# Optimization experiments

Hardware: AMD Instinct MI355X
Metric: run time of the kernel (lower is better)

## Reference

```python
import jax, jax.numpy as jnp
import numpy as np

HIDDEN = 2048
N_HEADS = 16
N_KV_HEADS = 4
HEAD_DIM = HIDDEN // N_HEADS  # 128
ROPE_THETA = 10000.0
BATCH = 2
SEQ = 2048


def setup_inputs() -> dict:
    key = jax.random.key(0)
    k1, k2, k3, k4, k5 = jax.random.split(key, 5)
    s = 0.02
    return {
        "hidden_states": jax.random.normal(k1, (BATCH, SEQ, HIDDEN), dtype=jnp.float32),
        "attention_mask": jnp.zeros((BATCH, 1, 1, SEQ), dtype=jnp.float32),
        "Wq": jax.random.normal(k2, (HIDDEN, N_HEADS * HEAD_DIM), dtype=jnp.float32) * s,
        "Wk": jax.random.normal(k3, (HIDDEN, N_KV_HEADS * HEAD_DIM), dtype=jnp.float32) * s,
        "Wv": jax.random.normal(k4, (HIDDEN, N_KV_HEADS * HEAD_DIM), dtype=jnp.float32) * s,
        "Wo": jax.random.normal(k5, (N_HEADS * HEAD_DIM, HIDDEN), dtype=jnp.float32) * s,
    }


def _rope_cos_sin(seq_len, dtype):
    inv_freq = 1.0 / (ROPE_THETA ** (jnp.arange(0, HEAD_DIM, 2, dtype=jnp.float32) / HEAD_DIM))
    t = jnp.arange(seq_len, dtype=jnp.float32)
    freqs = t[:, None] * inv_freq[None, :]            # [S, D/2]
    emb = jnp.concatenate([freqs, freqs], axis=-1)    # [S, D]
    cos = jnp.cos(emb)[None, None, :, :].astype(dtype)  # [1,1,S,D]
    sin = jnp.sin(emb)[None, None, :, :].astype(dtype)
    return cos, sin


def _apply_rope(x, cos, sin):
    # x: [B,H,S,D]; faithful to torch code: rotated = cat((-x[...,1::2], x[...,::2]), -1)
    x1 = x[..., ::2]
    x2 = x[..., 1::2]
    rotated = jnp.concatenate([-x2, x1], axis=-1)
    return x * cos + rotated * sin


def reference(hidden_states, attention_mask, Wq, Wk, Wv, Wo):
    B, S, _ = hidden_states.shape
    scale = HEAD_DIM ** -0.5

    q = (hidden_states @ Wq).reshape(B, S, N_HEADS, HEAD_DIM).transpose(0, 2, 1, 3)      # [B,H,S,D]
    k = (hidden_states @ Wk).reshape(B, S, N_KV_HEADS, HEAD_DIM).transpose(0, 2, 1, 3)   # [B,KV,S,D]
    v = (hidden_states @ Wv).reshape(B, S, N_KV_HEADS, HEAD_DIM).transpose(0, 2, 1, 3)

    cos, sin = _rope_cos_sin(S, hidden_states.dtype)
    q = _apply_rope(q, cos, sin)
    k = _apply_rope(k, cos, sin)

    rep = N_HEADS // N_KV_HEADS
    k = jnp.repeat(k, rep, axis=1)  # [B,H,S,D]
    v = jnp.repeat(v, rep, axis=1)

    scores = jnp.einsum("bhqd,bhkd->bhqk", q, k) * scale  # [B,H,S,S]
    causal = jnp.tril(jnp.ones((S, S), dtype=bool))[None, None]
    scores = jnp.where(causal, scores, -jnp.inf)
    scores = scores + attention_mask  # additive float mask, broadcast [B,1,1,S]

    attn = jax.nn.softmax(scores, axis=-1)
    out = jnp.einsum("bhqk,bhkd->bhqd", attn, v)           # [B,H,S,D]
    out = out.transpose(0, 2, 1, 3).reshape(B, S, N_HEADS * HEAD_DIM)
    return out @ Wo
```

## Files before the change

kernel.cpp:

```cpp
#include <hip/hip_runtime.h>
#include <hip/hip_bf16.h>

#define BATCH 2
#define SEQ   2048
#define NH    16
#define NKV   4
#define HD    128
#define KDIM  2048
#define MROWS 4096
#define NQKV  3072

typedef __attribute__((ext_vector_type(8))) short  s16x8;
typedef __attribute__((ext_vector_type(4))) short  s16x4;
typedef __attribute__((ext_vector_type(4))) float  f32x4;
typedef __attribute__((ext_vector_type(8))) __bf16 b16x8;

#define BARRIER_LDS() do { \
    asm volatile("s_waitcnt lgkmcnt(0)" ::: "memory"); \
    __builtin_amdgcn_s_barrier(); \
  } while (0)

__device__ __forceinline__ unsigned short f2bf(float f) {
  __hip_bfloat16 h = __float2bfloat16(f);
  return *reinterpret_cast<unsigned short*>(&h);
}
__device__ __forceinline__ float bf2f(unsigned short h) {
  union { unsigned int u; float f; } x; x.u = ((unsigned int)h) << 16;
  return x.f;
}

__device__ __forceinline__ unsigned pack2_trunc(float hif, float lof) {
  unsigned r, sel = 0x07060302u;
  asm("v_perm_b32 %0, %1, %2, %3" : "=v"(r) : "v"(hif), "v"(lof), "v"(sel));
  return r;
}
__device__ __forceinline__ float max3f(float a, float b, float c) {
  float r;
  asm("v_max3_f32 %0, %1, %2, %3" : "=v"(r) : "v"(a), "v"(b), "v"(c));
  return r;
}

__device__ __forceinline__ f32x4 MFMA16(s16x8 a, s16x8 b, f32x4 c) {
  return __builtin_amdgcn_mfma_f32_16x16x32_bf16(
      __builtin_bit_cast(b16x8, a), __builtin_bit_cast(b16x8, b), c, 0, 0, 0);
}

__device__ __forceinline__ void gload_lds16(const void* g, void* lds) {
  __builtin_amdgcn_global_load_lds(
      (const __attribute__((address_space(1))) void*)g,
      (__attribute__((address_space(3))) void*)lds, 16, 0, 0);
}

__global__ __launch_bounds__(256) void prep_all(
    const float* __restrict__ hidden,
    const float* __restrict__ Wq, const float* __restrict__ Wk,
    const float* __restrict__ Wv, const float* __restrict__ Wo,
    const float* __restrict__ mask,
    unsigned short* __restrict__ Ab, unsigned short* __restrict__ BT,
    unsigned short* __restrict__ WoT, float* __restrict__ tbl,
    float* __restrict__ maskS) {
  __shared__ float tile[32][33];
  int bid = blockIdx.x;
  if (bid < 10240) {
    int sub = bid % 160, ky = bid / 160;
    const float* W; unsigned short* WT; int Nd, nb;
    if (sub < 64)       { W = Wq; WT = BT;                       Nd = 2048; nb = sub; }
    else if (sub < 80)  { W = Wk; WT = BT + (size_t)2048 * KDIM; Nd = 512;  nb = sub - 64; }
    else if (sub < 96)  { W = Wv; WT = BT + (size_t)2560 * KDIM; Nd = 512;  nb = sub - 80; }
    else                { W = Wo; WT = WoT;                      Nd = 2048; nb = sub - 96; }
    int n0 = nb * 32, k0 = ky * 32;
    int tx = threadIdx.x & 31, ty = threadIdx.x >> 5;
#pragma unroll
    for (int i = 0; i < 4; ++i)
      tile[ty + i * 8][tx] = W[(size_t)(k0 + ty + i * 8) * Nd + n0 + tx];
    __syncthreads();
#pragma unroll
    for (int i = 0; i < 4; ++i)
      WT[(size_t)(n0 + ty + i * 8) * KDIM + k0 + tx] = f2bf(tile[tx][ty + i * 8]);
  } else if (bid < 14336) {
    int i = (bid - 10240) * 256 + threadIdx.x;
    const float4 a = ((const float4*)hidden)[2 * i];
    const float4 b = ((const float4*)hidden)[2 * i + 1];
    s16x8 o;
    o[0] = (short)f2bf(a.x); o[1] = (short)f2bf(a.y);
    o[2] = (short)f2bf(a.z); o[3] = (short)f2bf(a.w);
    o[4] = (short)f2bf(b.x); o[5] = (short)f2bf(b.y);
    o[6] = (short)f2bf(b.z); o[7] = (short)f2bf(b.w);
    ((s16x8*)Ab)[i] = o;
  } else if (bid < 14848) {
    int i = (bid - 14336) * 256 + threadIdx.x;
    int s = i >> 6, j = i & 63;
    float inv = powf(10000.0f, -(float)(2 * j) * (1.0f / 128.0f));
    float f = (float)s * inv;
    tbl[2 * i]     = cosf(f);
    tbl[2 * i + 1] = sinf(f);
  } else {
    int i = (bid - 14848) * 256 + threadIdx.x;
    maskS[i] = mask[i] * 1.44269504088896f;
  }
}

__global__ __launch_bounds__(512, 2) void gemm_qkv(
    const unsigned short* __restrict__ A, const unsigned short* __restrict__ BT,
    const float* __restrict__ tbl,
    unsigned short* __restrict__ Qo, unsigned short* __restrict__ Ko,
    unsigned short* __restrict__ Vo) {
  __shared__ __align__(16) unsigned short lds_[66560];
#define RING(buf, ab) (lds_ + (((buf) * 2 + (ab)) << 13))
  int tid = threadIdx.x, lane = tid & 63;
  int w = tid >> 6, wm = w >> 2, wn = w & 3;
  int lin = blockIdx.x;
  int swz = (lin & 7) * 24 + (lin >> 3);
  int bx = swz % 12, by = swz / 12;
  int m0 = by * 256, n0 = bx * 256;
  int fr = lane & 15, cg4 = lane >> 4, rg4 = (lane >> 4) * 4;

  int rS1 = tid >> 2,        cS1 = (tid & 3) ^ (rS1 & 3);
  int t2  = tid + 512;
  int rS2 = t2 >> 2,         cS2 = (t2 & 3) ^ (rS2 & 3);

  f32x4 acc[8][4] = {};

#pragma unroll
  for (int kt = 0; kt < 2; ++kt) {
    gload_lds16(A + (size_t)(m0 + rS1) * KDIM + kt * 32 + cS1 * 8,
                (char*)RING(kt, 0) + (size_t)tid * 16);
    gload_lds16(A + (size_t)(m0 + rS2) * KDIM + kt * 32 + cS2 * 8,
                (char*)RING(kt, 0) + (size_t)t2 * 16);
    gload_lds16(BT + (size_t)(n0 + rS1) * KDIM + kt * 32 + cS1 * 8,
                (char*)RING(kt, 1) + (size_t)tid * 16);
    gload_lds16(BT + (size_t)(n0 + rS2) * KDIM + kt * 32 + cS2 * 8,
                (char*)RING(kt, 1) + (size_t)t2 * 16);
  }

  const int NK = KDIM / 32;
  for (int kt = 0; kt < NK; ++kt) {
    int buf = kt & 3;
    if (kt == NK - 1) asm volatile("s_waitcnt vmcnt(0)" ::: "memory");
    else              asm volatile("s_waitcnt vmcnt(4)" ::: "memory");
    __builtin_amdgcn_s_barrier();

    const unsigned short* lA = RING(buf, 0);
    const unsigned short* lB = RING(buf, 1);
    s16x8 bfr[4], afr[4];
#pragma unroll
    for (int nf = 0; nf < 4; ++nf) {
      int rb = wn * 64 + nf * 16 + fr;
      bfr[nf] = *(const s16x8*)(lB + rb * 32 + (cg4 ^ (rb & 3)) * 8);
    }
#pragma unroll
    for (int mf = 0; mf < 4; ++mf) {
      int ra = wm * 128 + mf * 16 + fr;
      afr[mf] = *(const s16x8*)(lA + ra * 32 + (cg4 ^ (ra & 3)) * 8);
    }
    if (kt + 2 < NK) {
      int nb = (kt + 2) & 3, ko = (kt + 2) * 32;
      gload_lds16(A + (size_t)(m0 + rS1) * KDIM + ko + cS1 * 8,
                  (char*)RING(nb, 0) + (size_t)tid * 16);
      gload_lds16(A + (size_t)(m0 + rS2) * KDIM + ko + cS2 * 8,
                  (char*)RING(nb, 0) + (size_t)t2 * 16);
    }
    __builtin_amdgcn_s_setprio(1);
#pragma unroll
    for (int mf = 0; mf < 4; ++mf)
#pragma unroll
      for (int nf = 0; nf < 4; ++nf)
        acc[mf][nf] = MFMA16(afr[mf], bfr[nf], acc[mf][nf]);
    __builtin_amdgcn_s_setprio(0);
#pragma unroll
    for (int mf = 0; mf < 4; ++mf) {
      int ra = wm * 128 + (mf + 4) * 16 + fr;
      afr[mf] = *(const s16x8*)(lA + ra * 32 + (cg4 ^ (ra & 3)) * 8);
    }
    if (kt + 2 < NK) {
      int nb = (kt + 2) & 3, ko = (kt + 2) * 32;
      gload_lds16(BT + (size_t)(n0 + rS1) * KDIM + ko + cS1 * 8,
                  (char*)RING(nb, 1) + (size_t)tid * 16);
      gload_lds16(BT + (size_t)(n0 + rS2) * KDIM + ko + cS2 * 8,
                  (char*)RING(nb, 1) + (size_t)t2 * 16);
    }
    __builtin_amdgcn_s_setprio(1);
#pragma unroll
    for (int mf = 0; mf < 4; ++mf)
#pragma unroll
      for (int nf = 0; nf < 4; ++nf)
        acc[mf + 4][nf] = MFMA16(afr[mf], bfr[nf], acc[mf + 4][nf]);
    __builtin_amdgcn_s_setprio(0);
  }

  if (bx < 10) {
    BARRIER_LDS();
    unsigned short* sc_ = lds_;
#pragma unroll
    for (int mf = 0; mf < 8; ++mf)
#pragma unroll
      for (int nf = 0; nf < 4; ++nf)
#pragma unroll
        for (int r = 0; r < 4; ++r)
          sc_[(wm * 128 + mf * 16 + rg4 + r) * 260 + wn * 64 + nf * 16 + fr] =
              f2bf(acc[mf][nf][r]);
    BARRIER_LDS();

#pragma unroll
    for (int i = 0; i < 8; ++i) {
      int t = tid + 512 * i;
      int row = t >> 4, rem = t & 15;
      int hl = rem >> 3, j0 = (rem & 7) * 8;
      int grow = m0 + row, bb = grow >> 11, ss = grow & 2047;
      const unsigned short* xb = sc_ + row * 260 + hl * 128;
      s16x8 xj  = *(const s16x8*)(xb + j0);
      s16x8 xj6 = *(const s16x8*)(xb + 64 + j0);
      s16x8 x2a = *(const s16x8*)(xb + 2 * j0);
      s16x8 x2b = *(const s16x8*)(xb + 2 * j0 + 8);
      const float* tb = tbl + ((size_t)ss * 64 + j0) * 2;
      union { float4 v[4]; float a[16]; } cs;
      cs.v[0] = *(const float4*)(tb);
      cs.v[1] = *(const float4*)(tb + 4);
      cs.v[2] = *(const float4*)(tb + 8);
      cs.v[3] = *(const float4*)(tb + 12);
      s16x8 o0, o1;
#pragma unroll
      for (int k = 0; k < 8; ++k) {
        float c  = cs.a[2 * k];
        float sn = cs.a[2 * k + 1];
        float xjf  = bf2f((unsigned short)xj[k]);
        float xj6f = bf2f((unsigned short)xj6[k]);
        float x2j  = (2 * k < 8) ? bf2f((unsigned short)x2a[2 * k])
                                 : bf2f((unsigned short)x2b[2 * k - 8]);
        float x2j1 = (2 * k + 1 < 8) ? bf2f((unsigned short)x2a[2 * k + 1])
                                     : bf2f((unsigned short)x2b[2 * k + 1 - 8]);
        o0[k] = (short)f2bf(xjf * c - x2j1 * sn);
        o1[k] = (short)f2bf(xj6f * c + x2j * sn);
      }
      unsigned short* dstp;
      if (bx < 8) {
        int hh = bx * 2 + hl;
        dstp = Qo + ((size_t)(bb * NH + hh) * SEQ + ss) * HD;
      } else {
        int kvh = (bx - 8) * 2 + hl;
        dstp = Ko + ((size_t)(bb * NKV + kvh) * SEQ + ss) * HD;
      }
      *(s16x8*)(dstp + j0)      = o0;
      *(s16x8*)(dstp + 64 + j0) = o1;
    }
  } else {
    int rbase = m0 + wm * 128 + rg4;
#pragma unroll
    for (int nf = 0; nf < 4; ++nf) {
      int gn = n0 + wn * 64 + nf * 16 + fr;
      int c = gn - 2560, kvh = c >> 7, d = c & 127;
#pragma unroll
      for (int mf = 0; mf < 8; ++mf) {
        int grow0 = rbase + mf * 16;
        int bb = grow0 >> 11, ss = grow0 & 2047;
        s16x4 pk;
#pragma unroll
        for (int r = 0; r < 4; ++r) pk[r] = (short)f2bf(acc[mf][nf][r]);
        *(s16x4*)(Vo + ((size_t)(bb * NKV + kvh) * HD + d) * SEQ + ss) = pk;
      }
    }
  }
#undef RING
}

__global__ __launch_bounds__(512, 1) void gemm_out(
    const unsigned short* __restrict__ A, const unsigned short* __restrict__ BT,
    float* __restrict__ C) {
  __shared__ __align__(16) unsigned short ldsA[4][8192];
  __shared__ __align__(16) unsigned short ldsB[4][4096];
  int tid = threadIdx.x, lane = tid & 63;
  int w = tid >> 6, wm = w >> 2, wn = w & 3;
  int lin = blockIdx.x;
  int swz = (lin & 7) * 32 + (lin >> 3);
  int bx = swz % 16, by = swz / 16;
  int m0 = by * 256, n0 = bx * 128;
  int fr = lane & 15, cg4 = lane >> 4, rg4 = (lane >> 4) * 4;

  int rS1 = tid >> 2,  cS1 = (tid & 3) ^ (rS1 & 3);
  int t2  = tid + 512;
  int rS2 = t2 >> 2,   cS2 = (t2 & 3) ^ (rS2 & 3);
  int rB  = tid >> 2,  cB  = (tid & 3) ^ (rB & 3);

  f32x4 acc[8][2] = {};

#pragma unroll
  for (int kt = 0; kt < 2; ++kt) {
    gload_lds16(A + (size_t)(m0 + rS1) * KDIM + kt * 32 + cS1 * 8,
                (char*)&ldsA[kt][0] + (size_t)tid * 16);
    gload_lds16(A + (size_t)(m0 + rS2) * KDIM + kt * 32 + cS2 * 8,
                (char*)&ldsA[kt][0] + (size_t)t2 * 16);
    gload_lds16(BT + (size_t)(n0 + rB) * KDIM + kt * 32 + cB * 8,
                (char*)&ldsB[kt][0] + (size_t)tid * 16);
  }

  const int NK = KDIM / 32;
  for (int kt = 0; kt < NK; ++kt) {
    int buf = kt & 3;
    if (kt == NK - 1) asm volatile("s_waitcnt vmcnt(0)" ::: "memory");
    else              asm volatile("s_waitcnt vmcnt(3)" ::: "memory");
    __builtin_amdgcn_s_barrier();

    const unsigned short* lA = &ldsA[buf][0];
    const unsigned short* lB = &ldsB[buf][0];
    s16x8 bfr[2], afr[4];
#pragma unroll
    for (int nf = 0; nf < 2; ++nf) {
      int rb = wn * 32 + nf * 16 + fr;
      bfr[nf] = *(const s16x8*)(lB + rb * 32 + (cg4 ^ (rb & 3)) * 8);
    }
#pragma unroll
    for (int mf = 0; mf < 4; ++mf) {
      int ra = wm * 128 + mf * 16 + fr;
      afr[mf] = *(const s16x8*)(lA + ra * 32 + (cg4 ^ (ra & 3)) * 8);
    }
    if (kt + 2 < NK) {
      int nb = (kt + 2) & 3, ko = (kt + 2) * 32;
      gload_lds16(A + (size_t)(m0 + rS1) * KDIM + ko + cS1 * 8,
                  (char*)&ldsA[nb][0] + (size_t)tid * 16);
      gload_lds16(A + (size_t)(m0 + rS2) * KDIM + ko + cS2 * 8,
                  (char*)&ldsA[nb][0] + (size_t)t2 * 16);
    }
    __builtin_amdgcn_s_setprio(1);
#pragma unroll
    for (int mf = 0; mf < 4; ++mf)
#pragma unroll
      for (int nf = 0; nf < 2; ++nf)
        acc[mf][nf] = MFMA16(afr[mf], bfr[nf], acc[mf][nf]);
    __builtin_amdgcn_s_setprio(0);
#pragma unroll
    for (int mf = 0; mf < 4; ++mf) {
      int ra = wm * 128 + (mf + 4) * 16 + fr;
      afr[mf] = *(const s16x8*)(lA + ra * 32 + (cg4 ^ (ra & 3)) * 8);
    }
    if (kt + 2 < NK) {
      int nb = (kt + 2) & 3, ko = (kt + 2) * 32;
      gload_lds16(BT + (size_t)(n0 + rB) * KDIM + ko + cB * 8,
                  (char*)&ldsB[nb][0] + (size_t)tid * 16);
    }
    __builtin_amdgcn_s_setprio(1);
#pragma unroll
    for (int mf = 0; mf < 4; ++mf)
#pragma unroll
      for (int nf = 0; nf < 2; ++nf)
        acc[mf + 4][nf] = MFMA16(afr[mf], bfr[nf], acc[mf + 4][nf]);
    __builtin_amdgcn_s_setprio(0);
  }

  int rbase = m0 + wm * 128 + rg4;
#pragma unroll
  for (int nf = 0; nf < 2; ++nf) {
    int gn = n0 + wn * 32 + nf * 16 + fr;
#pragma unroll
    for (int mf = 0; mf < 8; ++mf)
#pragma unroll
      for (int r = 0; r < 4; ++r)
        C[(size_t)(rbase + mf * 16 + r) * 2048 + gn] = acc[mf][nf][r];
  }
}

__global__ __launch_bounds__(256, 2) void attn_fwd(
    const unsigned short* __restrict__ Q, const unsigned short* __restrict__ K,
    const unsigned short* __restrict__ VT, const float* __restrict__ maskS,
    unsigned short* __restrict__ O) {
  __shared__ __align__(16) unsigned short kt_[2][64][136];
  __shared__ __align__(16) unsigned short vt_[2][128][68];
  __shared__ __align__(16) unsigned short pt_[4][16][36];

  int tid = threadIdx.x, lane = tid & 63, w = tid >> 6;
  int l = blockIdx.x;
  int grp = l & 7, slot = l >> 3;
  int hloc = slot & 3, qt = 31 - (slot >> 2);
  int b = grp >> 2, kvh = grp & 3, h = kvh * 4 + hloc;
  int qbase = qt * 64;
  int qw = qbase + w * 16;
  int fr = lane & 15, g = lane >> 4, kg = g * 8, rg = g * 4;

  const unsigned short* Qb = Q + (size_t)(b * NH + h) * SEQ * HD;
  const unsigned short* Kb = K + (size_t)(b * NKV + kvh) * SEQ * HD;
  const unsigned short* Vb = VT + (size_t)(b * NKV + kvh) * HD * SEQ;
  const float* mb = maskS + (size_t)b * SEQ;

  int krow = tid >> 4, kpos = (tid & 15) * 8;
  const float sc2 = 0.12751744584812722f;
  int bS = b * SEQ;
  int ntiles = qt + 1;

  s16x8 aq[4];
#pragma unroll
  for (int dc = 0; dc < 4; ++dc)
    aq[dc] = *(const s16x8*)(Qb + (size_t)(qw + fr) * HD + dc * 32 + kg);

  f32x4 oacc[8] = {};
  float m_r = -3e38f, l_r = 0.f;

  s16x8 kreg[4], vreg[4];
#pragma unroll
  for (int i = 0; i < 4; ++i)
    kreg[i] = *(const s16x8*)(Kb + (size_t)(krow + i * 16) * HD + kpos);
#pragma unroll
  for (int i = 0; i < 4; ++i) {
    int c = tid + 256 * i;
    vreg[i] = *(const s16x8*)(Vb + (size_t)(c >> 3) * SEQ + (c & 7) * 8);
  }
#pragma unroll
  for (int i = 0; i < 4; ++i)
    *(s16x8*)(&kt_[0][krow + i * 16][kpos]) = kreg[i];
#pragma unroll
  for (int i = 0; i < 4; ++i) {
    int c = tid + 256 * i;
    *(s16x8*)(&vt_[0][c >> 3][(c & 7) * 8]) = vreg[i];
  }
  if (ntiles > 1) {
#pragma unroll
    for (int i = 0; i < 4; ++i)
      kreg[i] = *(const s16x8*)(Kb + (size_t)(64 + krow + i * 16) * HD + kpos);
#pragma unroll
    for (int i = 0; i < 4; ++i) {
      int c = tid + 256 * i;
      vreg[i] = *(const s16x8*)(Vb + (size_t)(c >> 3) * SEQ + 64 + (c & 7) * 8);
    }
  }
  BARRIER_LDS();

  for (int t = 0; t < ntiles; ++t) {
    int kv0 = t * 64;
    int cur = t & 1;
    bool diag = (t == qt);

    if (t + 1 < ntiles) {
#pragma unroll
      for (int i = 0; i < 4; ++i)
        *(s16x8*)(&kt_[cur ^ 1][krow + i * 16][kpos]) = kreg[i];
#pragma unroll
      for (int i = 0; i < 4; ++i) {
        int c = tid + 256 * i;
        *(s16x8*)(&vt_[cur ^ 1][c >> 3][(c & 7) * 8]) = vreg[i];
      }
      if (t + 2 < ntiles) {
#pragma unroll
        for (int i = 0; i < 4; ++i)
          kreg[i] = *(const s16x8*)(Kb + (size_t)(kv0 + 128 + krow + i * 16) * HD + kpos);
#pragma unroll
        for (int i = 0; i < 4; ++i) {
          int c = tid + 256 * i;
          vreg[i] = *(const s16x8*)(Vb + (size_t)(c >> 3) * SEQ + kv0 + 128 + (c & 7) * 8);
        }
      }
    }

    f32x4 sf[4];
    __builtin_amdgcn_s_setprio(1);
#pragma unroll
    for (int mk = 0; mk < 4; ++mk) {
      s16x8 ak[4];
#pragma unroll
      for (int dc = 0; dc < 4; ++dc)
        ak[dc] = *(const s16x8*)(&kt_[cur][mk * 16 + fr][dc * 32 + kg]);
      sf[mk] = f32x4{0.f, 0.f, 0.f, 0.f};
#pragma unroll
      for (int dc = 0; dc < 4; ++dc)
        sf[mk] = MFMA16(ak[dc], aq[dc], sf[mk]);
    }
    __builtin_amdgcn_s_setprio(0);

#pragma unroll
    for (int mk = 0; mk < 4; ++mk) {
      float4 mv = *(const float4*)(mb + kv0 + mk * 16 + rg);
      float mvr[4] = {mv.x, mv.y, mv.z, mv.w};
      if (diag) {
#pragma unroll
        for (int r = 0; r < 4; ++r) {
          int kv = kv0 + mk * 16 + rg + r;
          float v = sf[mk][r] * sc2 + mvr[r];
          sf[mk][r] = (kv <= qw + fr) ? v : -3e38f;
        }
      } else {
#pragma unroll
        for (int r = 0; r < 4; ++r)
          sf[mk][r] = sf[mk][r] * sc2 + mvr[r];
      }
    }

    float m0_ = max3f(sf[0][0], sf[0][1], sf[0][2]);
    float m1_ = max3f(sf[0][3], sf[1][0], sf[1][1]);
    float m2_ = max3f(sf[1][2], sf[1][3], sf[2][0]);
    float m3_ = max3f(sf[2][1], sf[2][2], sf[2][3]);
    float m4_ = max3f(sf[3][0], sf[3][1], sf[3][2]);
    float ma_ = max3f(m0_, m1_, m2_);
    float mb_ = max3f(m3_, m4_, sf[3][3]);
    float pm = fmaxf(ma_, mb_);
    pm = fmaxf(pm, __shfl_xor(pm, 16, 64));
    pm = fmaxf(pm, __shfl_xor(pm, 32, 64));
    if (!__all(pm - m_r <= 8.0f)) {
      float mo = m_r;
      float mn = fmaxf(mo, pm);
      float al = exp2f(mo - mn);
      m_r = mn;
      l_r *= al;
#pragma unroll
      for (int r = 0; r < 4; ++r) {
        float ar = __shfl(al, rg + r, 16);
#pragma unroll
        for (int od = 0; od < 8; ++od) oacc[od][r] *= ar;
      }
    }
    float rs = 0.f;
#pragma unroll
    for (int mk = 0; mk < 4; ++mk)
#pragma unroll
      for (int r = 0; r < 4; ++r) {
        float ppv = exp2f(sf[mk][r] - m_r);
        sf[mk][r] = ppv;
        rs += ppv;
      }
    rs += __shfl_xor(rs, 16, 64);
    rs += __shfl_xor(rs, 32, 64);
    l_r += rs;

#pragma unroll
    for (int kk = 0; kk < 2; ++kk) {
#pragma unroll
      for (int mh = 0; mh < 2; ++mh) {
        int mk = kk * 2 + mh;
        unsigned w0 = pack2_trunc(sf[mk][1], sf[mk][0]);
        unsigned w1 = pack2_trunc(sf[mk][3], sf[mk][2]);
        uint2 pk2; pk2.x = w0; pk2.y = w1;
        *(uint2*)(&pt_[w][fr][mh * 16 + rg]) = pk2;
      }
      s16x8 ap = *(const s16x8*)(&pt_[w][fr][kg]);
      __builtin_amdgcn_s_setprio(1);
#pragma unroll
      for (int od = 0; od < 8; ++od) {
        s16x8 bv = *(const s16x8*)(&vt_[cur][od * 16 + fr][kk * 32 + kg]);
        oacc[od] = MFMA16(ap, bv, oacc[od]);
      }
      __builtin_amdgcn_s_setprio(0);
    }

    BARRIER_LDS();
  }

  float iv = 1.0f / l_r;
  float ivr[4];
#pragma unroll
  for (int r = 0; r < 4; ++r) ivr[r] = __shfl(iv, rg + r, 16);
#pragma unroll
  for (int r = 0; r < 4; ++r) {
    unsigned short* op = O + (size_t)(bS + qw + rg + r) * 2048 + h * 128 + fr;
#pragma unroll
    for (int od = 0; od < 8; ++od)
      op[od * 16] = f2bf(oacc[od][r] * ivr[r]);
  }
}

extern "C" void kernel_launch(void* const* d_in, const int* in_sizes, int n_in,
                              void* d_out, int out_size, void* d_ws, size_t ws_size,
                              hipStream_t stream) {
  const float* hidden = (const float*)d_in[0];
  const float* mask   = (const float*)d_in[1];
  const float* Wq     = (const float*)d_in[2];
  const float* Wk     = (const float*)d_in[3];
  const float* Wv     = (const float*)d_in[4];
  const float* Wo     = (const float*)d_in[5];
  float* out = (float*)d_out;

  char* ws = (char*)d_ws;
  unsigned short* BT  = (unsigned short*)(ws);
  unsigned short* WoT = (unsigned short*)(ws + 12582912);
  unsigned short* Qb  = (unsigned short*)(ws + 20971520);
  unsigned short* Kb  = (unsigned short*)(ws + 37748736);
  unsigned short* VT  = (unsigned short*)(ws + 41943040);
  unsigned short* AO  = (unsigned short*)(ws + 46137344);
  float*          tbl = (float*)(ws + 62914560);
  float*          mkS = (float*)(ws + 63963136);
  unsigned short* Ab  = AO;

  prep_all<<<dim3(14864), 256, 0, stream>>>(hidden, Wq, Wk, Wv, Wo, mask,
                                            Ab, BT, WoT, tbl, mkS);
  gemm_qkv<<<dim3(192), 512, 0, stream>>>(Ab, BT, tbl, Qb, Kb, VT);
  attn_fwd<<<dim3(1024), 256, 0, stream>>>(Qb, Kb, VT, mkS, AO);
  gemm_out<<<dim3(256), 512, 0, stream>>>(AO, WoT, out);
}
```

Baseline: 201.6 us.

## Load attention K/V tiles directly to LDS with XOR-swizzled layout

Replaces the register-staged K/V prefetch (global load into registers, then LDS store) with direct global-to-LDS loads (gload_lds16) into unpadded, XOR-swizzled tiles. Barriers now wait on vmcnt instead of lgkmcnt, and the LDS reads use the matching swizzled indices. This cuts register pressure and LDS store instructions and shrinks LDS use by dropping the padding. The prefetch distance drops from two tiles to one, so load latency is less hidden. The row-sum is also rewritten as a tree reduction.

After: 201.1 us. About the same (-0.2%).

```diff
diff --git a/kernel.cpp b/kernel.cpp
--- a/kernel.cpp
+++ b/kernel.cpp
@@ -17,6 +17,11 @@
 
 #define BARRIER_LDS() do { \
     asm volatile("s_waitcnt lgkmcnt(0)" ::: "memory"); \
+    __builtin_amdgcn_s_barrier(); \
+  } while (0)
+
+#define BARRIER_VM() do { \
+    asm volatile("s_waitcnt vmcnt(0)" ::: "memory"); \
     __builtin_amdgcn_s_barrier(); \
   } while (0)
 
@@ -362,8 +367,8 @@
     const unsigned short* __restrict__ Q, const unsigned short* __restrict__ K,
     const unsigned short* __restrict__ VT, const float* __restrict__ maskS,
     unsigned short* __restrict__ O) {
-  __shared__ __align__(16) unsigned short kt_[2][64][136];
-  __shared__ __align__(16) unsigned short vt_[2][128][68];
+  __shared__ __align__(16) unsigned short kt_[2][64 * 128];
+  __shared__ __align__(16) unsigned short vt_[2][128 * 64];
   __shared__ __align__(16) unsigned short pt_[4][16][36];
 
   int tid = threadIdx.x, lane = tid & 63, w = tid >> 6;
@@ -380,7 +385,6 @@
   const unsigned short* Vb = VT + (size_t)(b * NKV + kvh) * HD * SEQ;
   const float* mb = maskS + (size_t)b * SEQ;
 
-  int krow = tid >> 4, kpos = (tid & 15) * 8;
   const float sc2 = 0.12751744584812722f;
   int bS = b * SEQ;
   int ntiles = qt + 1;
@@ -393,34 +397,19 @@
   f32x4 oacc[8] = {};
   float m_r = -3e38f, l_r = 0.f;
 
-  s16x8 kreg[4], vreg[4];
-#pragma unroll
-  for (int i = 0; i < 4; ++i)
-    kreg[i] = *(const s16x8*)(Kb + (size_t)(krow + i * 16) * HD + kpos);
 #pragma unroll
   for (int i = 0; i < 4; ++i) {
-    int c = tid + 256 * i;
-    vreg[i] = *(const s16x8*)(Vb + (size_t)(c >> 3) * SEQ + (c & 7) * 8);
-  }
-#pragma unroll
-  for (int i = 0; i < 4; ++i)
-    *(s16x8*)(&kt_[0][krow + i * 16][kpos]) = kreg[i];
+    int s = tid + 256 * i;
+    int r = s >> 4, cg = (s & 15) ^ (r & 15);
+    gload_lds16(Kb + (size_t)r * HD + cg * 8, (char*)&kt_[0][0] + (size_t)s * 16);
+  }
 #pragma unroll
   for (int i = 0; i < 4; ++i) {
-    int c = tid + 256 * i;
-    *(s16x8*)(&vt_[0][c >> 3][(c & 7) * 8]) = vreg[i];
-  }
-  if (ntiles > 1) {
-#pragma unroll
-    for (int i = 0; i < 4; ++i)
-      kreg[i] = *(const s16x8*)(Kb + (size_t)(64 + krow + i * 16) * HD + kpos);
-#pragma unroll
-    for (int i = 0; i < 4; ++i) {
-      int c = tid + 256 * i;
-      vreg[i] = *(const s16x8*)(Vb + (size_t)(c >> 3) * SEQ + 64 + (c & 7) * 8);
-    }
-  }
-  BARRIER_LDS();
+    int s = tid + 256 * i;
+    int d = s >> 3, cg = (s & 7) ^ (d & 7);
+    gload_lds16(Vb + (size_t)d * SEQ + cg * 8, (char*)&vt_[0][0] + (size_t)s * 16);
+  }
+  BARRIER_VM();
 
   for (int t = 0; t < ntiles; ++t) {
     int kv0 = t * 64;
@@ -429,22 +418,18 @@
 
     if (t + 1 < ntiles) {
 #pragma unroll
-      for (int i = 0; i < 4; ++i)
-        *(s16x8*)(&kt_[cur ^ 1][krow + i * 16][kpos]) = kreg[i];
-#pragma unroll
       for (int i = 0; i < 4; ++i) {
-        int c = tid + 256 * i;
-        *(s16x8*)(&vt_[cur ^ 1][c >> 3][(c & 7) * 8]) = vreg[i];
-      }
-      if (t + 2 < ntiles) {
-#pragma unroll
-        for (int i = 0; i < 4; ++i)
-          kreg[i] = *(const s16x8*)(Kb + (size_t)(kv0 + 128 + krow + i * 16) * HD + kpos);
-#pragma unroll
-        for (int i = 0; i < 4; ++i) {
-          int c = tid + 256 * i;
-          vreg[i] = *(const s16x8*)(Vb + (size_t)(c >> 3) * SEQ + kv0 + 128 + (c & 7) * 8);
-        }
+        int s = tid + 256 * i;
+        int r = s >> 4, cg = (s & 15) ^ (r & 15);
+        gload_lds16(Kb + (size_t)(kv0 + 64 + r) * HD + cg * 8,
+                    (char*)&kt_[cur ^ 1][0] + (size_t)s * 16);
+      }
+#pragma unroll
+      for (int i = 0; i < 4; ++i) {
+        int s = tid + 256 * i;
+        int d = s >> 3, cg = (s & 7) ^ (d & 7);
+        gload_lds16(Vb + (size_t)d * SEQ + kv0 + 64 + cg * 8,
+                    (char*)&vt_[cur ^ 1][0] + (size_t)s * 16);
       }
     }
 
@@ -455,7 +440,7 @@
       s16x8 ak[4];
 #pragma unroll
       for (int dc = 0; dc < 4; ++dc)
-        ak[dc] = *(const s16x8*)(&kt_[cur][mk * 16 + fr][dc * 32 + kg]);
+        ak[dc] = *(const s16x8*)(&kt_[cur][((mk * 16 + fr) * 16 + ((dc * 4 + g) ^ fr)) * 8]);
       sf[mk] = f32x4{0.f, 0.f, 0.f, 0.f};
 #pragma unroll
       for (int dc = 0; dc < 4; ++dc)
@@ -504,15 +489,20 @@
         for (int od = 0; od < 8; ++od) oacc[od][r] *= ar;
       }
     }
-    float rs = 0.f;
+    float e[16];
 #pragma unroll
     for (int mk = 0; mk < 4; ++mk)
 #pragma unroll
       for (int r = 0; r < 4; ++r) {
         float ppv = exp2f(sf[mk][r] - m_r);
         sf[mk][r] = ppv;
-        rs += ppv;
-      }
+        e[mk * 4 + r] = ppv;
+      }
+    float s0 = (e[0] + e[1]) + (e[2] + e[3]);
+    float s1 = (e[4] + e[5]) + (e[6] + e[7]);
+    float s2 = (e[8] + e[9]) + (e[10] + e[11]);
+    float s3 = (e[12] + e[13]) + (e[14] + e[15]);
+    float rs = (s0 + s1) + (s2 + s3);
     rs += __shfl_xor(rs, 16, 64);
     rs += __shfl_xor(rs, 32, 64);
     l_r += rs;
@@ -531,13 +521,14 @@
       __builtin_amdgcn_s_setprio(1);
 #pragma unroll
       for (int od = 0; od < 8; ++od) {
-        s16x8 bv = *(const s16x8*)(&vt_[cur][od * 16 + fr][kk * 32 + kg]);
+        s16x8 bv = *(const s16x8*)(
+            &vt_[cur][((od * 16 + fr) * 8 + ((kk * 4 + g) ^ (fr & 7))) * 8]);
         oacc[od] = MFMA16(ap, bv, oacc[od]);
       }
       __builtin_amdgcn_s_setprio(0);
     }
 
-    BARRIER_LDS();
+    BARRIER_VM();
   }
 
   float iv = 1.0f / l_r;
```
